# Performance work log

Measured on AMD Instinct MI355X. Metric: run time of the kernel, lower is better.

## Reference

```python
import jax, jax.numpy as jnp
import numpy as np


def _rnn_layer(x, W_ih, W_hh, b_ih, b_hh):
    """PyTorch tanh RNN layer, batch_first. x: [B,T,I] -> out: [B,T,H].
    h_t = tanh(x_t @ W_ih.T + b_ih + h_{t-1} @ W_hh.T + b_hh), h_0 = 0.
    """
    B = x.shape[0]
    H = W_hh.shape[0]
    # precompute input contribution for all timesteps at once: [T,B,H]
    pre = jnp.einsum('bti,hi->tbh', x, W_ih) + b_ih + b_hh

    def step(h, pre_t):
        h_new = jnp.tanh(pre_t + h @ W_hh.T)
        return h_new, h_new

    h0 = jnp.zeros((B, H), dtype=x.dtype)
    _, out = jax.lax.scan(step, h0, pre)  # out: [T,B,H]
    return jnp.transpose(out, (1, 0, 2))  # [B,T,H]


def setup_inputs() -> dict:
    key = jax.random.key(0)
    ks = jax.random.split(key, 11)
    B, T, I, H = 2048, 512, 8, 64
    s_i = 1.0 / np.sqrt(H)
    return {
        'x': jax.random.normal(ks[0], (B, T, I), dtype=jnp.float32),
        'W_ih0': jax.random.normal(ks[1], (H, I), dtype=jnp.float32) * s_i,
        'W_hh0': jax.random.normal(ks[2], (H, H), dtype=jnp.float32) * s_i,
        'b_ih0': jax.random.normal(ks[3], (H,), dtype=jnp.float32) * s_i,
        'b_hh0': jax.random.normal(ks[4], (H,), dtype=jnp.float32) * s_i,
        'W_ih1': jax.random.normal(ks[5], (H, H), dtype=jnp.float32) * s_i,
        'W_hh1': jax.random.normal(ks[6], (H, H), dtype=jnp.float32) * s_i,
        'b_ih1': jax.random.normal(ks[7], (H,), dtype=jnp.float32) * s_i,
        'b_hh1': jax.random.normal(ks[8], (H,), dtype=jnp.float32) * s_i,
        'fc_w': jax.random.normal(ks[9], (1, H), dtype=jnp.float32) * s_i,
        'fc_b': jax.random.normal(ks[10], (1,), dtype=jnp.float32) * s_i,
    }


def reference(x, W_ih0, W_hh0, b_ih0, b_hh0, W_ih1, W_hh1, b_ih1, b_hh1, fc_w, fc_b):
    out0 = _rnn_layer(x, W_ih0, W_hh0, b_ih0, b_hh0)     # [B,T,H]
    out1 = _rnn_layer(out0, W_ih1, W_hh1, b_ih1, b_hh1)  # [B,T,H]
    last = out1[:, -1, :]                                # [B,H]
    return last @ fc_w.T + fc_b                          # [B,1]
```

## Files before the change

kernel.cpp:

```cpp
#include <hip/hip_runtime.h>

#define T_STEPS 512
#define BATCH   2048
#define HID     64
#define IN0     8
#define SPW     16
#define NBLK    (BATCH / SPW)
#define SS      8
#define NSS     (T_STEPS / SS)

typedef _Float16 h2 __attribute__((ext_vector_type(2)));
typedef _Float16 h4 __attribute__((ext_vector_type(4)));
typedef _Float16 h8 __attribute__((ext_vector_type(8)));
typedef float    f4 __attribute__((ext_vector_type(4)));

#define MFMA(a, b, c) __builtin_amdgcn_mfma_f32_16x16x32_f16((a), (b), (c), 0, 0, 0)

union F8 { h8 v; h2 p[4]; };
union H4U { h4 v; h2 p[2]; };
union H8U { h8 v; h4 h[2]; };

__device__ __forceinline__ h2 pkrtz(float a, float b) {
    return __builtin_bit_cast(h2, __builtin_amdgcn_cvt_pkrtz(a, b));
}

__device__ __forceinline__ float tanh_fast(float x) {
    float e = __builtin_amdgcn_exp2f(x * 2.885390081777927f);
    return 1.0f - 2.0f * __builtin_amdgcn_rcpf(e + 1.0f);
}

__device__ __forceinline__ h8 load_frag_f16(const float* Wrow) {
    const float4* p = (const float4*)Wrow;
    float4 a = p[0], b = p[1];
    F8 f; f.p[0] = pkrtz(a.x, a.y); f.p[1] = pkrtz(a.z, a.w);
          f.p[2] = pkrtz(b.x, b.y); f.p[3] = pkrtz(b.z, b.w);
    return f.v;
}

#define LDS_BARRIER() asm volatile("s_waitcnt lgkmcnt(0)\n\ts_barrier" ::: "memory")

__global__ __launch_bounds__(512, 1)
void rnn2_cf(const float* __restrict__ x,
             const float* __restrict__ Wih0, const float* __restrict__ Whh0,
             const float* __restrict__ bih0, const float* __restrict__ bhh0,
             const float* __restrict__ Wih1, const float* __restrict__ Whh1,
             const float* __restrict__ bih1, const float* __restrict__ bhh1,
             const float* __restrict__ fcw,  const float* __restrict__ fcb,
             float* __restrict__ out) {
    const int tid  = threadIdx.x;
    const int w    = tid >> 6;
    const int mt   = w & 3;
    const bool L0  = (w < 4);
    const int lane = tid & 63;
    const int n    = lane & 15;
    const int q    = lane >> 4;
    const int bseq = blockIdx.x * SPW;

    __shared__ __align__(16) h4 H0c[2][16][16];
    __shared__ __align__(16) h4 H1c[2][16][16];
    __shared__ float red[4][SPW];

    const int wc = 4 * mt + q;

    const f4 zero = {0.f, 0.f, 0.f, 0.f};
    const h2 z2 = pkrtz(0.f, 0.f);

    h8 wa[2], wb[2], wi0;
    f4 biasc, fcv;
    const int row = 16 * mt + n;
    if (L0) {
        #pragma unroll
        for (int kt = 0; kt < 2; ++kt)
            wa[kt] = load_frag_f16(Whh0 + row * HID + 32 * kt + 8 * q);
        const float2 ww = *(const float2*)(Wih0 + row * IN0 + 2 * q);
        F8 f; f.p[0] = pkrtz(ww.x, ww.y); f.p[1] = z2; f.p[2] = z2; f.p[3] = z2;
        wi0 = f.v;
        #pragma unroll
        for (int r = 0; r < 4; ++r) {
            const int i = 16 * mt + 4 * q + r;
            biasc[r] = bih0[i] + bhh0[i];
        }
    } else {
        #pragma unroll
        for (int kt = 0; kt < 2; ++kt) {
            wa[kt] = load_frag_f16(Wih1 + row * HID + 32 * kt + 8 * q);
            wb[kt] = load_frag_f16(Whh1 + row * HID + 32 * kt + 8 * q);
        }
        #pragma unroll
        for (int r = 0; r < 4; ++r) {
            const int i = 16 * mt + 4 * q + r;
            biasc[r] = bih1[i] + bhh1[i];
            fcv[r]   = fcw[i];
        }
    }
    const float fcb0 = fcb[0];

    const float* xrow = x + ((size_t)(bseq + n) * T_STEPS) * IN0 + 2 * q;

    h8 h0f[2] = {}, h1f[2] = {};
    f4 a0x;
    float2 xb[SS];
    if (L0) {
        const float2 x0 = *(const float2*)xrow;
        F8 xf; xf.p[0] = pkrtz(x0.x, x0.y); xf.p[1] = z2; xf.p[2] = z2; xf.p[3] = z2;
        a0x = MFMA(wi0, xf.v, biasc);
        #pragma unroll
        for (int i = 0; i < SS; ++i) {
            int tn = i + 1; if (tn > T_STEPS - 1) tn = T_STEPS - 1;
            xb[i] = *(const float2*)(xrow + tn * IN0);
        }
    }

    for (int s = 0; s < NSS; ++s) {
        #pragma unroll
        for (int i = 0; i < SS; ++i) {
            const int t = SS * s + i;
            const int bf = t & 1;
            if (L0) {
                f4 p0 = MFMA(wa[0], h0f[0], a0x);
                f4 p1 = MFMA(wa[1], h0f[1], zero);
                const f4 a0 = p0 + p1;
                H4U u;
                u.p[0] = pkrtz(tanh_fast(a0[0]), tanh_fast(a0[1]));
                u.p[1] = pkrtz(tanh_fast(a0[2]), tanh_fast(a0[3]));
                H0c[bf][wc][n] = u.v;
                F8 xf; xf.p[0] = pkrtz(xb[i].x, xb[i].y);
                xf.p[1] = z2; xf.p[2] = z2; xf.p[3] = z2;
                a0x = MFMA(wi0, xf.v, biasc);
                int tn = t + 1 + SS; if (tn > T_STEPS - 1) tn = T_STEPS - 1;
                xb[i] = *(const float2*)(xrow + tn * IN0);
            } else {
                f4 c0 = MFMA(wa[0], h0f[0], biasc);
                f4 c1 = MFMA(wa[1], h0f[1], zero);
                f4 c2 = MFMA(wb[0], h1f[0], zero);
                f4 c3 = MFMA(wb[1], h1f[1], zero);
                const f4 a1 = (c0 + c1) + (c2 + c3);
                H4U u;
                u.p[0] = pkrtz(tanh_fast(a1[0]), tanh_fast(a1[1]));
                u.p[1] = pkrtz(tanh_fast(a1[2]), tanh_fast(a1[3]));
                if (t == 0) { u.p[0] = z2; u.p[1] = z2; }
                H1c[bf][wc][n] = u.v;
            }
            LDS_BARRIER();
            {
                H8U b0, b1;
                b0.h[0] = H0c[bf][2 * q][n];     b0.h[1] = H0c[bf][2 * q + 1][n];
                b1.h[0] = H0c[bf][8 + 2 * q][n]; b1.h[1] = H0c[bf][9 + 2 * q][n];
                h0f[0] = b0.v; h0f[1] = b1.v;
            }
            if (!L0) {
                H8U b0, b1;
                b0.h[0] = H1c[bf][2 * q][n];     b0.h[1] = H1c[bf][2 * q + 1][n];
                b1.h[0] = H1c[bf][8 + 2 * q][n]; b1.h[1] = H1c[bf][9 + 2 * q][n];
                h1f[0] = b0.v; h1f[1] = b1.v;
            }
        }
    }

    if (!L0) {
        f4 c0 = MFMA(wa[0], h0f[0], biasc);
        f4 c1 = MFMA(wa[1], h0f[1], zero);
        f4 c2 = MFMA(wb[0], h1f[0], zero);
        f4 c3 = MFMA(wb[1], h1f[1], zero);
        const f4 a1 = (c0 + c1) + (c2 + c3);
        float sacc = 0.f;
        #pragma unroll
        for (int r = 0; r < 4; ++r) sacc += fcv[r] * tanh_fast(a1[r]);
        sacc += __shfl_xor(sacc, 16, 64);
        sacc += __shfl_xor(sacc, 32, 64);
        if (lane < 16) red[mt][n] = sacc;
    }
    __syncthreads();
    if (tid < SPW)
        out[bseq + tid] = red[0][tid] + red[1][tid] + red[2][tid] + red[3][tid] + fcb0;
}

extern "C" void kernel_launch(void* const* d_in, const int* in_sizes, int n_in,
                              void* d_out, int out_size, void* d_ws, size_t ws_size,
                              hipStream_t stream) {
    const float* x    = (const float*)d_in[0];
    const float* Wih0 = (const float*)d_in[1];
    const float* Whh0 = (const float*)d_in[2];
    const float* bih0 = (const float*)d_in[3];
    const float* bhh0 = (const float*)d_in[4];
    const float* Wih1 = (const float*)d_in[5];
    const float* Whh1 = (const float*)d_in[6];
    const float* bih1 = (const float*)d_in[7];
    const float* bhh1 = (const float*)d_in[8];
    const float* fcw  = (const float*)d_in[9];
    const float* fcb  = (const float*)d_in[10];
    float* out = (float*)d_out;

    rnn2_cf<<<dim3(NBLK), dim3(512), 0, stream>>>(
        x, Wih0, Whh0, bih0, bhh0, Wih1, Whh1, bih1, bhh1, fcw, fcb, out);
}
```

Before: 235.4 us.

## Lag layer-1 by one extra step and pack hidden-state LDS layout into h8

Layer-1 waves now consume layer-0's hidden state from the previous buffer, one step behind. Each h0 value is read in the step after it was written, so the layer-0 loads no longer sit right after the barrier on layer 1's critical path. The LDS layout is repacked so each MFMA operand fragment is a single h8 load instead of two h4 loads. Layer-0 waves get raised scheduling priority around their recurrent chain. An extra drain step and a barrier are added at the end to finish the lagged pipeline.

```diff
diff --git a/kernel.cpp b/kernel.cpp
--- a/kernel.cpp
+++ b/kernel.cpp
@@ -18,7 +18,6 @@
 
 union F8 { h8 v; h2 p[4]; };
 union H4U { h4 v; h2 p[2]; };
-union H8U { h8 v; h4 h[2]; };
 
 __device__ __forceinline__ h2 pkrtz(float a, float b) {
     return __builtin_bit_cast(h2, __builtin_amdgcn_cvt_pkrtz(a, b));
@@ -40,13 +39,13 @@
 #define LDS_BARRIER() asm volatile("s_waitcnt lgkmcnt(0)\n\ts_barrier" ::: "memory")
 
 __global__ __launch_bounds__(512, 1)
-void rnn2_cf(const float* __restrict__ x,
-             const float* __restrict__ Wih0, const float* __restrict__ Whh0,
-             const float* __restrict__ bih0, const float* __restrict__ bhh0,
-             const float* __restrict__ Wih1, const float* __restrict__ Whh1,
-             const float* __restrict__ bih1, const float* __restrict__ bhh1,
-             const float* __restrict__ fcw,  const float* __restrict__ fcb,
-             float* __restrict__ out) {
+void rnn2_lag(const float* __restrict__ x,
+              const float* __restrict__ Wih0, const float* __restrict__ Whh0,
+              const float* __restrict__ bih0, const float* __restrict__ bhh0,
+              const float* __restrict__ Wih1, const float* __restrict__ Whh1,
+              const float* __restrict__ bih1, const float* __restrict__ bhh1,
+              const float* __restrict__ fcw,  const float* __restrict__ fcb,
+              float* __restrict__ out) {
     const int tid  = threadIdx.x;
     const int w    = tid >> 6;
     const int mt   = w & 3;
@@ -56,11 +55,12 @@
     const int q    = lane >> 4;
     const int bseq = blockIdx.x * SPW;
 
-    __shared__ __align__(16) h4 H0c[2][16][16];
-    __shared__ __align__(16) h4 H1c[2][16][16];
+    __shared__ __align__(16) h8 H0p[2][8][16];
+    __shared__ __align__(16) h8 H1p[2][8][16];
     __shared__ float red[4][SPW];
 
-    const int wc = 4 * mt + q;
+    const int wp  = 2 * mt + (q >> 1);
+    const int ws  = q & 1;
 
     const f4 zero = {0.f, 0.f, 0.f, 0.f};
     const h2 z2 = pkrtz(0.f, 0.f);
@@ -97,7 +97,7 @@
 
     const float* xrow = x + ((size_t)(bseq + n) * T_STEPS) * IN0 + 2 * q;
 
-    h8 h0f[2] = {}, h1f[2] = {};
+    h8 h0f[2] = {}, h0n[2] = {}, h1f[2] = {};
     f4 a0x;
     float2 xb[SS];
     if (L0) {
@@ -109,6 +109,7 @@
             int tn = i + 1; if (tn > T_STEPS - 1) tn = T_STEPS - 1;
             xb[i] = *(const float2*)(xrow + tn * IN0);
         }
+        __builtin_amdgcn_s_setprio(1);
     }
 
     for (int s = 0; s < NSS; ++s) {
@@ -123,46 +124,61 @@
                 H4U u;
                 u.p[0] = pkrtz(tanh_fast(a0[0]), tanh_fast(a0[1]));
                 u.p[1] = pkrtz(tanh_fast(a0[2]), tanh_fast(a0[3]));
-                H0c[bf][wc][n] = u.v;
+                ((h4*)&H0p[bf][wp][n])[ws] = u.v;
+                __builtin_amdgcn_s_setprio(0);
                 F8 xf; xf.p[0] = pkrtz(xb[i].x, xb[i].y);
                 xf.p[1] = z2; xf.p[2] = z2; xf.p[3] = z2;
                 a0x = MFMA(wi0, xf.v, biasc);
                 int tn = t + 1 + SS; if (tn > T_STEPS - 1) tn = T_STEPS - 1;
                 xb[i] = *(const float2*)(xrow + tn * IN0);
             } else {
-                f4 c0 = MFMA(wa[0], h0f[0], biasc);
-                f4 c1 = MFMA(wa[1], h0f[1], zero);
+                f4 c0 = MFMA(wa[0], h0n[0], biasc);
+                f4 c1 = MFMA(wa[1], h0n[1], zero);
                 f4 c2 = MFMA(wb[0], h1f[0], zero);
                 f4 c3 = MFMA(wb[1], h1f[1], zero);
                 const f4 a1 = (c0 + c1) + (c2 + c3);
                 H4U u;
                 u.p[0] = pkrtz(tanh_fast(a1[0]), tanh_fast(a1[1]));
                 u.p[1] = pkrtz(tanh_fast(a1[2]), tanh_fast(a1[3]));
-                if (t == 0) { u.p[0] = z2; u.p[1] = z2; }
-                H1c[bf][wc][n] = u.v;
+                if (t < 2) { u.p[0] = z2; u.p[1] = z2; }
+                ((h4*)&H1p[bf][wp][n])[ws] = u.v;
+                h0n[0] = H0p[bf ^ 1][q][n];
+                h0n[1] = H0p[bf ^ 1][4 + q][n];
             }
             LDS_BARRIER();
-            {
-                H8U b0, b1;
-                b0.h[0] = H0c[bf][2 * q][n];     b0.h[1] = H0c[bf][2 * q + 1][n];
-                b1.h[0] = H0c[bf][8 + 2 * q][n]; b1.h[1] = H0c[bf][9 + 2 * q][n];
-                h0f[0] = b0.v; h0f[1] = b1.v;
+            if (L0) {
+                __builtin_amdgcn_s_setprio(1);
+                h0f[0] = H0p[bf][q][n];
+                h0f[1] = H0p[bf][4 + q][n];
+            } else {
+                h1f[0] = H1p[bf][q][n];
+                h1f[1] = H1p[bf][4 + q][n];
             }
-            if (!L0) {
-                H8U b0, b1;
-                b0.h[0] = H1c[bf][2 * q][n];     b0.h[1] = H1c[bf][2 * q + 1][n];
-                b1.h[0] = H1c[bf][8 + 2 * q][n]; b1.h[1] = H1c[bf][9 + 2 * q][n];
-                h1f[0] = b0.v; h1f[1] = b1.v;
-            }
         }
     }
 
     if (!L0) {
-        f4 c0 = MFMA(wa[0], h0f[0], biasc);
-        f4 c1 = MFMA(wa[1], h0f[1], zero);
-        f4 c2 = MFMA(wb[0], h1f[0], zero);
-        f4 c3 = MFMA(wb[1], h1f[1], zero);
-        const f4 a1 = (c0 + c1) + (c2 + c3);
+        f4 e0 = MFMA(wa[0], h0n[0], biasc);
+        f4 e1 = MFMA(wa[1], h0n[1], zero);
+        f4 e2 = MFMA(wb[0], h1f[0], zero);
+        f4 e3 = MFMA(wb[1], h1f[1], zero);
+        const f4 aA = (e0 + e1) + (e2 + e3);
+        H4U u;
+        u.p[0] = pkrtz(tanh_fast(aA[0]), tanh_fast(aA[1]));
+        u.p[1] = pkrtz(tanh_fast(aA[2]), tanh_fast(aA[3]));
+        ((h4*)&H1p[0][wp][n])[ws] = u.v;
+    } else {
+        __builtin_amdgcn_s_setprio(0);
+    }
+    LDS_BARRIER();
+    if (!L0) {
+        const h8 hx0 = H0p[1][q][n],  hx1 = H0p[1][4 + q][n];
+        const h8 g0  = H1p[0][q][n],  g1  = H1p[0][4 + q][n];
+        f4 f0 = MFMA(wa[0], hx0, biasc);
+        f4 f1 = MFMA(wa[1], hx1, zero);
+        f4 f2 = MFMA(wb[0], g0, zero);
+        f4 f3 = MFMA(wb[1], g1, zero);
+        const f4 a1 = (f0 + f1) + (f2 + f3);
         float sacc = 0.f;
         #pragma unroll
         for (int r = 0; r < 4; ++r) sacc += fcv[r] * tanh_fast(a1[r]);
@@ -191,6 +207,6 @@
     const float* fcb  = (const float*)d_in[10];
     float* out = (float*)d_out;
 
-    rnn2_cf<<<dim3(NBLK), dim3(512), 0, stream>>>(
+    rnn2_lag<<<dim3(NBLK), dim3(512), 0, stream>>>(
         x, Wih0, Whh0, bih0, bhh0, Wih1, Whh1, bih1, bhh1, fcw, fcb, out);
 }
```

Result: no change. 236.5 us (+0.5%).

## Decouple RNN layers into producer/consumer blocks linked by global ring buffers

Applied to the files above, without the earlier changes.

Layer 0 and layer 1 now run in separate 256-thread blocks, one pair per 16-sequence tile. Layer 0 streams its hidden states into a 32-slot global ring buffer with flag-based flow control, and layer 1 prefetches 8 steps at a time so it can run up to a ring's worth behind. The aim is to remove the lockstep coupling, where the layer-1 waves wait on the layer-0 recurrence each step, and to double the number of blocks. The cost is a memset launch, global-memory traffic and spin waits. If producer and consumer blocks are not co-resident, progress depends on the spin cap, which risks deadlock or wrong results.

```diff
diff --git a/kernel.cpp b/kernel.cpp
--- a/kernel.cpp
+++ b/kernel.cpp
@@ -5,20 +5,29 @@
 #define HID     64
 #define IN0     8
 #define SPW     16
+#define NPAIR   (BATCH / SPW)
 #define NBLK    (BATCH / SPW)
 #define SS      8
 #define NSS     (T_STEPS / SS)
+#define RSLOT   32
+#define RING_U64 (RSLOT * 256)
+#define DATA_OFF 65536
+#define FLAG_STRIDE 256
+#define WS_NEEDED ((size_t)DATA_OFF + (size_t)NPAIR * (RING_U64 * 8))
+#define SPIN_CAP  (1 << 18)
 
 typedef _Float16 h2 __attribute__((ext_vector_type(2)));
 typedef _Float16 h4 __attribute__((ext_vector_type(4)));
 typedef _Float16 h8 __attribute__((ext_vector_type(8)));
 typedef float    f4 __attribute__((ext_vector_type(4)));
+typedef unsigned long long u64;
 
 #define MFMA(a, b, c) __builtin_amdgcn_mfma_f32_16x16x32_f16((a), (b), (c), 0, 0, 0)
 
-union F8 { h8 v; h2 p[4]; };
+union F8  { h8 v; h2 p[4]; };
 union H4U { h4 v; h2 p[2]; };
 union H8U { h8 v; h4 h[2]; };
+union H4B { h4 v; u64 b; };
 
 __device__ __forceinline__ h2 pkrtz(float a, float b) {
     return __builtin_bit_cast(h2, __builtin_amdgcn_cvt_pkrtz(a, b));
@@ -38,6 +47,197 @@
 }
 
 #define LDS_BARRIER() asm volatile("s_waitcnt lgkmcnt(0)\n\ts_barrier" ::: "memory")
+
+#define ALOAD(p)     __hip_atomic_load((p),  __ATOMIC_RELAXED, __HIP_MEMORY_SCOPE_AGENT)
+#define ASTORE(p, v) __hip_atomic_store((p), (v), __ATOMIC_RELAXED, __HIP_MEMORY_SCOPE_AGENT)
+
+__global__ __launch_bounds__(256, 1)
+void rnn2_decoup(const float* __restrict__ x,
+                 const float* __restrict__ Wih0, const float* __restrict__ Whh0,
+                 const float* __restrict__ bih0, const float* __restrict__ bhh0,
+                 const float* __restrict__ Wih1, const float* __restrict__ Whh1,
+                 const float* __restrict__ bih1, const float* __restrict__ bhh1,
+                 const float* __restrict__ fcw,  const float* __restrict__ fcb,
+                 float* __restrict__ out, void* __restrict__ ws) {
+    const int tid  = threadIdx.x;
+    const int mt   = tid >> 6;
+    const int lane = tid & 63;
+    const int n    = lane & 15;
+    const int q    = lane >> 4;
+    const bool isL0 = (blockIdx.x < NPAIR);
+    const int pair  = isL0 ? blockIdx.x : blockIdx.x - NPAIR;
+    const int bseq  = pair * SPW;
+
+    int* prodp = (int*)((char*)ws + (size_t)pair * FLAG_STRIDE);
+    int* consp = (int*)((char*)ws + (size_t)pair * FLAG_STRIDE + 128);
+    u64* ring  = (u64*)((char*)ws + DATA_OFF + (size_t)pair * (RING_U64 * 8));
+
+    __shared__ __align__(16) h4 Hc[2][16][16];
+    __shared__ float red[4][SPW];
+
+    const int wc = 4 * mt + q;
+    const f4 zero = {0.f, 0.f, 0.f, 0.f};
+    const h2 z2 = pkrtz(0.f, 0.f);
+    const int row = 16 * mt + n;
+    const float fcb0 = fcb[0];
+
+    if (isL0) {
+        h8 wa[2], wi0;
+        f4 biasc;
+        #pragma unroll
+        for (int kt = 0; kt < 2; ++kt)
+            wa[kt] = load_frag_f16(Whh0 + row * HID + 32 * kt + 8 * q);
+        {
+            const float2 ww = *(const float2*)(Wih0 + row * IN0 + 2 * q);
+            F8 f; f.p[0] = pkrtz(ww.x, ww.y); f.p[1] = z2; f.p[2] = z2; f.p[3] = z2;
+            wi0 = f.v;
+        }
+        #pragma unroll
+        for (int r = 0; r < 4; ++r) {
+            const int i = 16 * mt + 4 * q + r;
+            biasc[r] = bih0[i] + bhh0[i];
+        }
+
+        const float* xrow = x + ((size_t)(bseq + n) * T_STEPS) * IN0 + 2 * q;
+        h8 h0f[2] = {};
+        f4 a0x;
+        float2 xb[SS];
+        {
+            const float2 x0 = *(const float2*)xrow;
+            F8 xf; xf.p[0] = pkrtz(x0.x, x0.y); xf.p[1] = z2; xf.p[2] = z2; xf.p[3] = z2;
+            a0x = MFMA(wi0, xf.v, biasc);
+            #pragma unroll
+            for (int i = 0; i < SS; ++i) {
+                int tn = i + 1; if (tn > T_STEPS - 1) tn = T_STEPS - 1;
+                xb[i] = *(const float2*)(xrow + tn * IN0);
+            }
+        }
+
+        for (int s = 0; s < NSS; ++s) {
+            if (lane == 0) {
+                int it = 0;
+                while (ALOAD(consp) < 8 * s - (RSLOT - SS) && it++ < SPIN_CAP)
+                    __builtin_amdgcn_s_sleep(2);
+            }
+            #pragma unroll
+            for (int i = 0; i < SS; ++i) {
+                const int t = SS * s + i;
+                const int bf = i & 1;
+                f4 p0 = MFMA(wa[0], h0f[0], a0x);
+                f4 p1 = MFMA(wa[1], h0f[1], zero);
+                const f4 a0 = p0 + p1;
+                H4U u;
+                u.p[0] = pkrtz(tanh_fast(a0[0]), tanh_fast(a0[1]));
+                u.p[1] = pkrtz(tanh_fast(a0[2]), tanh_fast(a0[3]));
+                Hc[bf][wc][n] = u.v;
+                { H4B bb; bb.v = u.v;
+                  ASTORE(ring + (size_t)(t & (RSLOT - 1)) * 256 + wc * 16 + n, bb.b); }
+                F8 xf; xf.p[0] = pkrtz(xb[i].x, xb[i].y);
+                xf.p[1] = z2; xf.p[2] = z2; xf.p[3] = z2;
+                a0x = MFMA(wi0, xf.v, biasc);
+                int tn = t + 1 + SS; if (tn > T_STEPS - 1) tn = T_STEPS - 1;
+                xb[i] = *(const float2*)(xrow + tn * IN0);
+
+                if (i == SS - 1) asm volatile("s_waitcnt vmcnt(0)" ::: "memory");
+                LDS_BARRIER();
+                if (i == SS - 1 && mt == 0 && lane == 0)
+                    ASTORE(prodp, t + 1);
+                H8U b0, b1;
+                b0.h[0] = Hc[bf][2 * q][n];     b0.h[1] = Hc[bf][2 * q + 1][n];
+                b1.h[0] = Hc[bf][8 + 2 * q][n]; b1.h[1] = Hc[bf][9 + 2 * q][n];
+                h0f[0] = b0.v; h0f[1] = b1.v;
+            }
+        }
+        return;
+    }
+
+    h8 wa[2], wb[2];
+    f4 biasc, fcv;
+    #pragma unroll
+    for (int kt = 0; kt < 2; ++kt) {
+        wa[kt] = load_frag_f16(Wih1 + row * HID + 32 * kt + 8 * q);
+        wb[kt] = load_frag_f16(Whh1 + row * HID + 32 * kt + 8 * q);
+    }
+    #pragma unroll
+    for (int r = 0; r < 4; ++r) {
+        const int i = 16 * mt + 4 * q + r;
+        biasc[r] = bih1[i] + bhh1[i];
+        fcv[r]   = fcw[i];
+    }
+
+    h8 h1f[2] = {};
+    f4 th = {0.f, 0.f, 0.f, 0.f};
+    h8 pA0[SS], pA1[SS], pB0[SS], pB1[SS];
+
+    auto spin_prod = [&](int tgt) {
+        if (lane == 0) {
+            int it = 0;
+            while (ALOAD(prodp) < tgt && it++ < SPIN_CAP)
+                __builtin_amdgcn_s_sleep(2);
+        }
+    };
+    auto l1_load = [&](h8 (&P0)[SS], h8 (&P1)[SS], int g) {
+        #pragma unroll
+        for (int i = 0; i < SS; ++i) {
+            const u64* rp = ring + (size_t)((g * SS + i) & (RSLOT - 1)) * 256;
+            H4B va, vb, vc, vd;
+            va.b = ALOAD(rp + (2 * q) * 16 + n);
+            vb.b = ALOAD(rp + (2 * q + 1) * 16 + n);
+            vc.b = ALOAD(rp + (8 + 2 * q) * 16 + n);
+            vd.b = ALOAD(rp + (9 + 2 * q) * 16 + n);
+            H8U f0, f1;
+            f0.h[0] = va.v; f0.h[1] = vb.v;
+            f1.h[0] = vc.v; f1.h[1] = vd.v;
+            P0[i] = f0.v; P1[i] = f1.v;
+        }
+    };
+    auto l1_group = [&](h8 (&P0)[SS], h8 (&P1)[SS]) {
+        #pragma unroll
+        for (int i = 0; i < SS; ++i) {
+            const int bf = i & 1;
+            f4 c0 = MFMA(wa[0], P0[i], biasc);
+            f4 c1 = MFMA(wa[1], P1[i], zero);
+            f4 c2 = MFMA(wb[0], h1f[0], zero);
+            f4 c3 = MFMA(wb[1], h1f[1], zero);
+            const f4 a1 = (c0 + c1) + (c2 + c3);
+            th[0] = tanh_fast(a1[0]); th[1] = tanh_fast(a1[1]);
+            th[2] = tanh_fast(a1[2]); th[3] = tanh_fast(a1[3]);
+            H4U u;
+            u.p[0] = pkrtz(th[0], th[1]);
+            u.p[1] = pkrtz(th[2], th[3]);
+            Hc[bf][wc][n] = u.v;
+            LDS_BARRIER();
+            H8U b0, b1;
+            b0.h[0] = Hc[bf][2 * q][n];     b0.h[1] = Hc[bf][2 * q + 1][n];
+            b1.h[0] = Hc[bf][8 + 2 * q][n]; b1.h[1] = Hc[bf][9 + 2 * q][n];
+            h1f[0] = b0.v; h1f[1] = b1.v;
+        }
+    };
+
+    spin_prod(SS);
+    l1_load(pA0, pA1, 0);
+    for (int G2 = 0; G2 < NSS / 2; ++G2) {
+        const int g = 2 * G2;
+        spin_prod(8 * (g + 2));
+        l1_load(pB0, pB1, g + 1);
+        l1_group(pA0, pA1);
+        if (mt == 0 && lane == 0) ASTORE(consp, 8 * (g + 1));
+        if (g + 2 < NSS) {
+            spin_prod(8 * (g + 3));
+            l1_load(pA0, pA1, g + 2);
+        }
+        l1_group(pB0, pB1);
+        if (mt == 0 && lane == 0) ASTORE(consp, 8 * (g + 2));
+    }
+
+    float sacc = th[0] * fcv[0] + th[1] * fcv[1] + th[2] * fcv[2] + th[3] * fcv[3];
+    sacc += __shfl_xor(sacc, 16, 64);
+    sacc += __shfl_xor(sacc, 32, 64);
+    if (lane < 16) red[mt][n] = sacc;
+    __syncthreads();
+    if (tid < SPW)
+        out[bseq + tid] = red[0][tid] + red[1][tid] + red[2][tid] + red[3][tid] + fcb0;
+}
 
 __global__ __launch_bounds__(512, 1)
 void rnn2_cf(const float* __restrict__ x,
@@ -61,7 +261,6 @@
     __shared__ float red[4][SPW];
 
     const int wc = 4 * mt + q;
-
     const f4 zero = {0.f, 0.f, 0.f, 0.f};
     const h2 z2 = pkrtz(0.f, 0.f);
 
@@ -191,6 +390,12 @@
     const float* fcb  = (const float*)d_in[10];
     float* out = (float*)d_out;
 
-    rnn2_cf<<<dim3(NBLK), dim3(512), 0, stream>>>(
-        x, Wih0, Whh0, bih0, bhh0, Wih1, Whh1, bih1, bhh1, fcw, fcb, out);
-}
+    if (d_ws != nullptr && ws_size >= WS_NEEDED) {
+        hipMemsetAsync(d_ws, 0, NPAIR * FLAG_STRIDE, stream);
+        rnn2_decoup<<<dim3(2 * NPAIR), dim3(256), 0, stream>>>(
+            x, Wih0, Whh0, bih0, bhh0, Wih1, Whh1, bih1, bhh1, fcw, fcb, out, d_ws);
+    } else {
+        rnn2_cf<<<dim3(NBLK), dim3(512), 0, stream>>>(
+            x, Wih0, Whh0, bih0, bhh0, Wih1, Whh1, bih1, bhh1, fcw, fcb, out);
+    }
+}
```

Measured after the change: 289.1 us. +22.8%, slower.
